# Kernel tuning notes

Measured on AMD Instinct MI355X. Metric: run time of the kernel, lower is better.

Reference implementation:

```python
import jax, jax.numpy as jnp
import numpy as np

N, E, C, NE, G, T = 20000, 320000, 32, 10, 64, 1000
NB, HID, LAYERS = 8, 64, 2
R_MAX, P_CUT, AVG_NEIGH = 5.0, 6, 16.0
LM = 16  # (max_ell+1)^2 spherical-harmonic components
L_OF_LM = jnp.array([0,1,1,1,2,2,2,2,2,3,3,3,3,3,3,3])


def sph_harm(u):
    # component-normalized real spherical harmonics up to l=3 on unit vectors u [E,3]
    x, y, z = u[:, 0], u[:, 1], u[:, 2]
    s3, s15, s5, s105, s7 = 3**0.5, 15**0.5, 5**0.5, 105**0.5, 7**0.5
    s35_8, s21_8 = (35.0/8.0)**0.5, (21.0/8.0)**0.5
    comps = [jnp.ones_like(x),
             s3*x, s3*y, s3*z,
             s15*x*y, s15*y*z, 0.5*s5*(3*z*z-1.0), s15*x*z, 0.5*s15*(x*x-y*y),
             s35_8*y*(3*x*x-y*y), s105*x*y*z, s21_8*y*(5*z*z-1.0),
             0.5*s7*(5*z*z*z-3*z), s21_8*x*(5*z*z-1.0),
             0.5*s105*z*(x*x-y*y), s35_8*x*(x*x-3*y*y)]
    return jnp.stack(comps, axis=-1)  # [E,16]


def radial_embed(r):
    # Bessel basis with polynomial cutoff (MACE RadialEmbeddingBlock)
    n = jnp.arange(1, NB + 1, dtype=r.dtype)
    rc = jnp.maximum(r, 1e-9)
    bessel = (2.0/R_MAX)**0.5 * jnp.sin(n[None, :]*jnp.pi*rc[:, None]/R_MAX) / rc[:, None]
    xr = r / R_MAX
    p = float(P_CUT)
    f = (1.0 - 0.5*(p+1)*(p+2)*xr**p + p*(p+2)*xr**(p+1) - 0.5*p*(p+1)*xr**(p+2))
    f = f * (xr < 1.0)
    return bessel * f[:, None]  # [E,NB]


def setup_inputs():
    key = jax.random.key(0)
    ks = jax.random.split(key, 16)
    positions = jax.random.normal(ks[0], (N, 3)) * 3.0
    species = jax.random.randint(ks[1], (N,), 0, NE)
    node_attrs = jax.nn.one_hot(species, NE, dtype=jnp.float32)
    edge_index = jax.random.randint(ks[2], (2, E), 0, N)
    shifts = jnp.zeros((E, 3), jnp.float32)
    batch = jnp.sort(jax.random.randint(ks[3], (N,), 0, G))
    t = jax.random.randint(ks[4], (G,), 0, T)
    eps = jax.random.normal(ks[5], (N, NE + 3))
    betas = jnp.linspace(1e-4, 0.02, T)
    alpha_bar = jnp.cumprod(1.0 - betas)
    sc = 0.1
    W_embed = sc * jax.random.normal(ks[6], (NE + 1, C))
    W_r1 = sc * jax.random.normal(ks[7], (LAYERS, NB, HID))
    W_r2 = sc * jax.random.normal(ks[8], (LAYERS, HID, C * 4))
    W_mix = sc * jax.random.normal(ks[9], (LAYERS, 4, C, C))
    W_sc = sc * jax.random.normal(ks[10], (NE, C))
    W_prod = sc * jax.random.normal(ks[11], (LAYERS, 3, C))
    W_ro_s = sc * jax.random.normal(ks[12], (LAYERS, C, NE))
    W_ro_v = sc * jax.random.normal(ks[13], (LAYERS, C))
    return {"positions": positions, "node_attrs": node_attrs, "shifts": shifts,
            "eps": eps, "alpha_bar": alpha_bar, "W_embed": W_embed, "W_r1": W_r1,
            "W_r2": W_r2, "W_mix": W_mix, "W_sc": W_sc, "W_prod": W_prod,
            "W_ro_s": W_ro_s, "W_ro_v": W_ro_v, "edge_index": edge_index,
            "batch": batch, "t": t}


def reference(positions, node_attrs, shifts, eps, alpha_bar, W_embed, W_r1, W_r2,
              W_mix, W_sc, W_prod, W_ro_s, W_ro_v, edge_index, batch, t):
    sender, receiver = edge_index[0], edge_index[1]
    # diffusion: noise positions and attrs (DDPM q(x_t|x_0))
    ab = alpha_bar[t][batch][:, None]                       # [N,1]
    attrs0 = node_attrs / 4.0
    pos_noisy = jnp.sqrt(ab) * positions + jnp.sqrt(1.0 - ab) * eps[:, -3:]
    attrs_noisy = jnp.sqrt(ab) * attrs0 + jnp.sqrt(1.0 - ab) * eps[:, :NE]
    tf = (t.astype(jnp.float32) / T)[batch][:, None]
    h = jnp.concatenate([attrs_noisy, tf], axis=-1) @ W_embed  # [N,C]
    # edge geometry
    vec = pos_noisy[receiver] - pos_noisy[sender] + shifts
    r = jnp.sqrt(jnp.sum(vec * vec, axis=-1) + 1e-12)
    Y = sph_harm(vec / r[:, None])                          # [E,16]
    ef = radial_embed(r)                                    # [E,NB]
    scalar = h
    pred = jnp.zeros((N, NE + 3), h.dtype)
    for layer in range(LAYERS):
        rw = jax.nn.silu(ef @ W_r1[layer]) @ W_r2[layer]    # [E,4C]
        rw = rw.reshape(E, C, 4)[:, :, L_OF_LM]             # [E,C,16]
        msg = rw * scalar[sender][:, :, None] * Y[:, None, :]
        agg = jax.ops.segment_sum(msg, receiver, num_segments=N) / AVG_NEIGH
        Wm = W_mix[layer][L_OF_LM]                          # [16,C,C]
        feats = jnp.einsum('nck,kcd->ndk', agg, Wm)         # per-l channel mix
        s = feats[:, :, 0]
        poly = W_prod[layer, 0] + W_prod[layer, 1] * s + W_prod[layer, 2] * s * s
        feats = feats * poly[:, :, None]                    # correlation-3 product
        if layer == 0:
            feats = feats.at[:, :, 0].add(attrs_noisy @ W_sc)  # element skip
        scalar = feats[:, :, 0]
        pred_s = scalar @ W_ro_s[layer]                     # [N,NE]
        pred_v = jnp.einsum('ncm,c->nm', feats[:, :, 1:4], W_ro_v[layer])  # [N,3]
        pred = pred + jnp.concatenate([pred_s, pred_v], axis=-1)
    err = (pred - eps) ** 2
    loss_pos = jax.ops.segment_sum(err[:, -3:].sum(-1), batch, num_segments=G)
    loss_lab = jax.ops.segment_sum(err[:, :NE].sum(-1), batch, num_segments=G)
    nn = jax.ops.segment_sum(jnp.ones((N,), pred.dtype), batch, num_segments=G)
    loss = 0.5 * (loss_pos + loss_lab) / (jnp.maximum(nn, 1.0) * (3 + NE))
    return loss
```

## Files before the change

kernel.cpp:

```cpp
#include <hip/hip_runtime.h>

typedef unsigned short ushort_t;
typedef unsigned int uint_t;

#define NN 20000
#define EE 320000
#define CC 32
#define NEL 10
#define GG 64
#define TTT 1000
#define NBB 8
#define HIDD 64
#define EPB 256

typedef __attribute__((ext_vector_type(8))) short bf16x8;
typedef __attribute__((ext_vector_type(4))) float f32x4;

__device__ __forceinline__ float bits2f(uint_t b) { union { uint_t u; float f; } v; v.u = b; return v.f; }
__device__ __forceinline__ ushort_t f2b(float f) {
  union { float f; uint_t u; } v; v.f = f;
  uint_t r = (v.u + 0x7fffu + ((v.u >> 16) & 1u)) >> 16;
  return (ushort_t)r;
}
__device__ __forceinline__ uint_t pk(float a, float b) {
  return (uint_t)f2b(a) | ((uint_t)f2b(b) << 16);
}
__device__ __forceinline__ float lo16(uint_t u) { return bits2f(u << 16); }
__device__ __forceinline__ float hi16(uint_t u) { return bits2f(u & 0xffff0000u); }

__global__ __launch_bounds__(256) void k_prep(
    const float* __restrict__ positions, const float* __restrict__ node_attrs,
    const float* __restrict__ eps, const float* __restrict__ alpha_bar,
    const float* __restrict__ W_embed, const float* __restrict__ W_sc,
    const int* __restrict__ batch, const int* __restrict__ tarr,
    float* __restrict__ pos_noisy, float* __restrict__ scalA,
    float* __restrict__ sc_skip, float* __restrict__ pred, int* __restrict__ deg)
{
  int n = blockIdx.x * 256 + threadIdx.x;
  if (n >= NN) return;
  deg[n] = 0;
  int g = batch[n];
  int tn = tarr[g];
  float ab = alpha_bar[tn];
  float sa = sqrtf(ab), sb = sqrtf(fmaxf(1.0f - ab, 0.0f));
#pragma unroll
  for (int j = 0; j < 3; ++j)
    pos_noisy[n * 3 + j] = sa * positions[n * 3 + j] + sb * eps[n * 13 + 10 + j];
  float an[10];
#pragma unroll
  for (int j = 0; j < 10; ++j)
    an[j] = sa * 0.25f * node_attrs[n * 10 + j] + sb * eps[n * 13 + j];
  float tf = (float)tn * (1.0f / (float)TTT);
  for (int d = 0; d < CC; ++d) {
    float h = tf * W_embed[10 * CC + d];
    float sk = 0.0f;
#pragma unroll
    for (int j = 0; j < 10; ++j) {
      h = fmaf(an[j], W_embed[j * CC + d], h);
      sk = fmaf(an[j], W_sc[j * CC + d], sk);
    }
    scalA[n * CC + d] = h;
    sc_skip[n * CC + d] = sk;
  }
#pragma unroll
  for (int j = 0; j < 13; ++j) pred[n * 13 + j] = 0.0f;
}

__global__ __launch_bounds__(256) void k_edge_deg(const int* __restrict__ ei,
    int* __restrict__ deg)
{
  int e = blockIdx.x * 256 + threadIdx.x;
  atomicAdd(&deg[ei[EE + e]], 1);
}

__global__ __launch_bounds__(1024) void k_scan(const int* __restrict__ deg,
    int* __restrict__ offs, int* __restrict__ cursor,
    float* __restrict__ lnum, float* __restrict__ lcnt)
{
  __shared__ int wsums[16];
  __shared__ int woffs[16];
  int tid = threadIdx.x, lane = tid & 63, wv = tid >> 6;
  if (tid < GG) { lnum[tid] = 0.0f; lcnt[tid] = 0.0f; }
  int base = tid * 20;
  int loc[20];
  int s = 0;
#pragma unroll
  for (int j = 0; j < 20; ++j) {
    int idx = base + j;
    int v = (idx < NN) ? deg[idx] : 0;
    loc[j] = s; s += v;
  }
  int inc = s;
  for (int o = 1; o < 64; o <<= 1) {
    int v = __shfl_up(inc, o, 64);
    if (lane >= o) inc += v;
  }
  if (lane == 63) wsums[wv] = inc;
  __syncthreads();
  if (wv == 0 && lane < 16) {
    int v = wsums[lane];
    int i2 = v;
    for (int o = 1; o < 16; o <<= 1) {
      int vv = __shfl_up(i2, o, 16);
      if (lane >= o) i2 += vv;
    }
    woffs[lane] = i2 - v;
  }
  __syncthreads();
  int texcl = woffs[wv] + (inc - s);
#pragma unroll
  for (int j = 0; j < 20; ++j) {
    int idx = base + j;
    if (idx < NN) { int v = texcl + loc[j]; offs[idx] = v; cursor[idx] = v; }
  }
  if (tid == 1023) offs[NN] = EE;
}

__global__ __launch_bounds__(256) void k_edge2(
    const float* __restrict__ pos_noisy, const float* __restrict__ shifts,
    const int* __restrict__ ei, int* __restrict__ cursor,
    ushort_t* __restrict__ Ys, ushort_t* __restrict__ efs, int* __restrict__ snds)
{
  int e = blockIdx.x * 256 + threadIdx.x;
  int snd = ei[e], rcv = ei[EE + e];
  float vx = pos_noisy[rcv * 3 + 0] - pos_noisy[snd * 3 + 0] + shifts[e * 3 + 0];
  float vy = pos_noisy[rcv * 3 + 1] - pos_noisy[snd * 3 + 1] + shifts[e * 3 + 1];
  float vz = pos_noisy[rcv * 3 + 2] - pos_noisy[snd * 3 + 2] + shifts[e * 3 + 2];
  float r2 = vx * vx + vy * vy + vz * vz + 1e-12f;
  float r = sqrtf(r2);
  float inv = 1.0f / r;
  float x = vx * inv, y = vy * inv, z = vz * inv;

  const float s3 = 1.7320508075688772f, s15 = 3.872983346207417f, s5 = 2.23606797749979f;
  const float s105 = 10.246950765959598f, s7 = 2.6457513110645907f;
  const float s35_8 = 2.091650066335189f, s21_8 = 1.6201851746019651f;
  float yv[16];
  yv[0] = 1.0f;
  yv[1] = s3 * x; yv[2] = s3 * y; yv[3] = s3 * z;
  yv[4] = s15 * x * y;
  yv[5] = s15 * y * z;
  yv[6] = 0.5f * s5 * (3.0f * z * z - 1.0f);
  yv[7] = s15 * x * z;
  yv[8] = 0.5f * s15 * (x * x - y * y);
  yv[9] = s35_8 * y * (3.0f * x * x - y * y);
  yv[10] = s105 * x * y * z;
  yv[11] = s21_8 * y * (5.0f * z * z - 1.0f);
  yv[12] = 0.5f * s7 * (5.0f * z * z * z - 3.0f * z);
  yv[13] = s21_8 * x * (5.0f * z * z - 1.0f);
  yv[14] = 0.5f * s105 * z * (x * x - y * y);
  yv[15] = s35_8 * x * (x * x - 3.0f * y * y);

  float rc = fmaxf(r, 1e-9f);
  float pref = 0.6324555320336759f / rc;
  float th = 0.6283185307179586f * rc;
  float s1 = __sinf(th), c1 = __cosf(th);
  float xr = r * 0.2f;
  float fcut = 0.0f;
  if (xr < 1.0f) {
    float x2 = xr * xr, x3 = x2 * xr;
    float x6 = x3 * x3, x7 = x6 * xr, x8 = x7 * xr;
    fcut = 1.0f - 28.0f * x6 + 48.0f * x7 - 21.0f * x8;
  }
  float efv[8];
  float sp = 0.0f, scur = s1, c2 = 2.0f * c1;
#pragma unroll
  for (int b = 0; b < 8; ++b) {
    efv[b] = pref * scur * fcut;
    float nx = c2 * scur - sp;
    sp = scur; scur = nx;
  }

  int slot = atomicAdd(&cursor[rcv], 1);
  snds[slot] = snd;
  uint4* Y4 = (uint4*)Ys;
  Y4[(size_t)slot * 2 + 0] = make_uint4(pk(yv[0], yv[1]), pk(yv[2], yv[3]),
                                        pk(yv[4], yv[5]), pk(yv[6], yv[7]));
  Y4[(size_t)slot * 2 + 1] = make_uint4(pk(yv[8], yv[9]), pk(yv[10], yv[11]),
                                        pk(yv[12], yv[13]), pk(yv[14], yv[15]));
  ((uint4*)efs)[slot] = make_uint4(pk(efv[0], efv[1]), pk(efv[2], efv[3]),
                                   pk(efv[4], efv[5]), pk(efv[6], efv[7]));
}

__global__ __launch_bounds__(256) void k_rw_mfma(
    const ushort_t* __restrict__ efs, const float* __restrict__ W_r1,
    const float* __restrict__ W_r2, ushort_t* __restrict__ rwc, int layer)
{
  __shared__ __align__(16) ushort_t w2t[128][72];
  __shared__ __align__(16) ushort_t h1[EPB][72];
  int tid = threadIdx.x;
  const float* W1g = W_r1 + layer * NBB * HIDD;
  const float* W2g = W_r2 + layer * HIDD * 128;
  for (int idx = tid; idx < HIDD * 128; idx += 256) {
    int k = idx >> 7, n = idx & 127;
    w2t[n][k] = f2b(W2g[idx]);
  }
  {
    int e = blockIdx.x * EPB + tid;
    uint4 q = ((const uint4*)efs)[e];
    float efr[8] = {lo16(q.x), hi16(q.x), lo16(q.y), hi16(q.y),
                    lo16(q.z), hi16(q.z), lo16(q.w), hi16(q.w)};
    for (int hc = 0; hc < 8; ++hc) {
      float v[8];
#pragma unroll
      for (int hh = 0; hh < 8; ++hh) {
        int h = hc * 8 + hh;
        float t = 0.0f;
#pragma unroll
        for (int b = 0; b < 8; ++b) t = fmaf(efr[b], W1g[b * HIDD + h], t);
        v[hh] = t / (1.0f + __expf(-t));
      }
      *(uint4*)&h1[tid][hc * 8] = make_uint4(pk(v[0], v[1]), pk(v[2], v[3]),
                                             pk(v[4], v[5]), pk(v[6], v[7]));
    }
  }
  __syncthreads();
  int w = tid >> 6, lane = tid & 63;
  int c = lane & 15, quad = lane >> 4;
  bf16x8 bfr[16];
#pragma unroll
  for (int nt = 0; nt < 8; ++nt)
#pragma unroll
    for (int kt = 0; kt < 2; ++kt)
      bfr[nt * 2 + kt] = *(const bf16x8*)&w2t[nt * 16 + c][kt * 32 + quad * 8];
  int mb0 = w * 64;
#pragma unroll
  for (int mt = 0; mt < 4; ++mt) {
    int mbase = mb0 + mt * 16;
    bf16x8 a0 = *(const bf16x8*)&h1[mbase + c][quad * 8];
    bf16x8 a1 = *(const bf16x8*)&h1[mbase + c][32 + quad * 8];
    size_t erow = (size_t)blockIdx.x * EPB + mbase + quad * 4;
#pragma unroll
    for (int nt = 0; nt < 8; ++nt) {
      f32x4 acc = {0.0f, 0.0f, 0.0f, 0.0f};
      acc = __builtin_amdgcn_mfma_f32_16x16x32_bf16(a0, bfr[nt * 2 + 0], acc, 0, 0, 0);
      acc = __builtin_amdgcn_mfma_f32_16x16x32_bf16(a1, bfr[nt * 2 + 1], acc, 0, 0, 0);
      int col = nt * 16 + c;
#pragma unroll
      for (int r = 0; r < 4; ++r)
        rwc[(erow + r) * 128 + col] = f2b(acc[r]);
    }
  }
}

__global__ __launch_bounds__(256) void k_layer(
    const ushort_t* __restrict__ Ys, const ushort_t* __restrict__ rwc,
    const int* __restrict__ snds,
    const float* __restrict__ scal_in, float* __restrict__ scal_out,
    const int* __restrict__ offs,
    const float* __restrict__ W_mix, const float* __restrict__ W_prod,
    const float* __restrict__ W_ro_s, const float* __restrict__ W_ro_v,
    const float* __restrict__ sc_skip, float* __restrict__ pred, int layer)
{
  __shared__ float lagg[4][CC][16];
  __shared__ float lf[4][CC][4];
  int w = threadIdx.x >> 6, lane = threadIdx.x & 63;
  int n = blockIdx.x * 4 + w;
  int c = lane >> 1;
  int kh = lane & 1;
  int kb = kh * 8;
  int i0 = offs[n], i1 = offs[n + 1];
  float acc0 = 0, acc1 = 0, acc2 = 0, acc3 = 0, acc4 = 0, acc5 = 0, acc6 = 0, acc7 = 0;
  const uint4* Y4 = (const uint4*)Ys;
  const uint2* rw2 = (const uint2*)rwc;
  for (int s = i0; s < i1; ++s) {
    uint4 q = Y4[(size_t)s * 2 + kh];
    uint2 rp = rw2[(size_t)s * 32 + c];
    float ss = scal_in[snds[s] * CC + c];
    float r0 = lo16(rp.x), r1 = hi16(rp.x), r2v = lo16(rp.y), r3 = hi16(rp.y);
    float w0 = kh ? r2v : r0;
    float w13 = kh ? r3 : r1;
    float w47 = kh ? r3 : r2v;
    float ya0 = lo16(q.x), ya1 = hi16(q.x), ya2 = lo16(q.y), ya3 = hi16(q.y);
    float yb0 = lo16(q.z), yb1 = hi16(q.z), yb2 = lo16(q.w), yb3 = hi16(q.w);
    acc0 = fmaf(w0 * ss, ya0, acc0);
    acc1 = fmaf(w13 * ss, ya1, acc1);
    acc2 = fmaf(w13 * ss, ya2, acc2);
    acc3 = fmaf(w13 * ss, ya3, acc3);
    acc4 = fmaf(w47 * ss, yb0, acc4);
    acc5 = fmaf(w47 * ss, yb1, acc5);
    acc6 = fmaf(w47 * ss, yb2, acc6);
    acc7 = fmaf(w47 * ss, yb3, acc7);
  }
  const float invavg = 1.0f / 16.0f;
  lagg[w][c][kb + 0] = acc0 * invavg;
  lagg[w][c][kb + 1] = acc1 * invavg;
  lagg[w][c][kb + 2] = acc2 * invavg;
  lagg[w][c][kb + 3] = acc3 * invavg;
  lagg[w][c][kb + 4] = acc4 * invavg;
  lagg[w][c][kb + 5] = acc5 * invavg;
  lagg[w][c][kb + 6] = acc6 * invavg;
  lagg[w][c][kb + 7] = acc7 * invavg;
  __syncthreads();
  int d = c;
  float ft[8] = {0, 0, 0, 0, 0, 0, 0, 0};
  const float* Wm = W_mix + layer * 4096;
  for (int cc2 = 0; cc2 < CC; ++cc2) {
    float m0 = Wm[cc2 * CC + d];
    float m1 = Wm[1024 + cc2 * CC + d];
    float m2 = Wm[2048 + cc2 * CC + d];
    float m3 = Wm[3072 + cc2 * CC + d];
    float u0 = kh ? m2 : m0;
    float u13 = kh ? m3 : m1;
    float u47 = kh ? m3 : m2;
    ft[0] = fmaf(lagg[w][cc2][kb + 0], u0, ft[0]);
    ft[1] = fmaf(lagg[w][cc2][kb + 1], u13, ft[1]);
    ft[2] = fmaf(lagg[w][cc2][kb + 2], u13, ft[2]);
    ft[3] = fmaf(lagg[w][cc2][kb + 3], u13, ft[3]);
    ft[4] = fmaf(lagg[w][cc2][kb + 4], u47, ft[4]);
    ft[5] = fmaf(lagg[w][cc2][kb + 5], u47, ft[5]);
    ft[6] = fmaf(lagg[w][cc2][kb + 6], u47, ft[6]);
    ft[7] = fmaf(lagg[w][cc2][kb + 7], u47, ft[7]);
  }
  float s = __shfl(ft[0], lane & 62, 64);
  const float* Wp = W_prod + layer * 96;
  float p0 = Wp[d], p1 = Wp[32 + d], p2 = Wp[64 + d];
  float poly = fmaf(fmaf(p2, s, p1), s, p0);
#pragma unroll
  for (int j = 0; j < 8; ++j) ft[j] *= poly;
  if (layer == 0 && kh == 0) ft[0] += sc_skip[n * CC + d];
  if (kh == 0) {
    scal_out[n * CC + d] = ft[0];
    lf[w][d][0] = ft[0]; lf[w][d][1] = ft[1]; lf[w][d][2] = ft[2]; lf[w][d][3] = ft[3];
  }
  __syncthreads();
  if (lane < 13) {
    float sum = 0.0f;
    if (lane < 10) {
      const float* Wr = W_ro_s + layer * CC * NEL;
      for (int dd = 0; dd < CC; ++dd) sum = fmaf(lf[w][dd][0], Wr[dd * NEL + lane], sum);
    } else {
      int mm = lane - 10;
      const float* Wv = W_ro_v + layer * CC;
      for (int dd = 0; dd < CC; ++dd) sum = fmaf(lf[w][dd][1 + mm], Wv[dd], sum);
    }
    pred[n * 13 + lane] += sum;
  }
}

__global__ __launch_bounds__(256) void k_loss(const float* __restrict__ pred,
    const float* __restrict__ eps, const int* __restrict__ batch,
    float* __restrict__ lnum, float* __restrict__ lcnt)
{
  __shared__ float psum[GG];
  __shared__ int pcnt[GG];
  int tid = threadIdx.x;
  if (tid < GG) { psum[tid] = 0.0f; pcnt[tid] = 0; }
  __syncthreads();
  int n = blockIdx.x * 256 + tid;
  if (n < NN) {
    int g = batch[n];
    float sum = 0.0f;
#pragma unroll
    for (int j = 0; j < 13; ++j) {
      float dlt = pred[n * 13 + j] - eps[n * 13 + j];
      sum = fmaf(dlt, dlt, sum);
    }
    atomicAdd(&psum[g], sum);
    atomicAdd(&pcnt[g], 1);
  }
  __syncthreads();
  if (tid < GG && pcnt[tid] > 0) {
    atomicAdd(&lnum[tid], psum[tid]);
    atomicAdd(&lcnt[tid], (float)pcnt[tid]);
  }
}

__global__ void k_final(const float* __restrict__ lnum, const float* __restrict__ lcnt,
    float* __restrict__ out)
{
  int g = threadIdx.x;
  if (g < GG) {
    float nn = fmaxf(lcnt[g], 1.0f);
    out[g] = 0.5f * lnum[g] / (nn * 13.0f);
  }
}

extern "C" void kernel_launch(void* const* d_in, const int* in_sizes, int n_in,
                              void* d_out, int out_size, void* d_ws, size_t ws_size,
                              hipStream_t stream) {
  const float* positions  = (const float*)d_in[0];
  const float* node_attrs = (const float*)d_in[1];
  const float* shifts     = (const float*)d_in[2];
  const float* eps        = (const float*)d_in[3];
  const float* alpha_bar  = (const float*)d_in[4];
  const float* W_embed    = (const float*)d_in[5];
  const float* W_r1       = (const float*)d_in[6];
  const float* W_r2       = (const float*)d_in[7];
  const float* W_mix      = (const float*)d_in[8];
  const float* W_sc       = (const float*)d_in[9];
  const float* W_prod     = (const float*)d_in[10];
  const float* W_ro_s     = (const float*)d_in[11];
  const float* W_ro_v     = (const float*)d_in[12];
  const int* edge_index   = (const int*)d_in[13];
  const int* batch        = (const int*)d_in[14];
  const int* tarr         = (const int*)d_in[15];
  float* out = (float*)d_out;

  char* ws = (char*)d_ws;
  size_t off = 0;
  auto alloc = [&](size_t bytes) -> void* {
    void* p = ws + off;
    off = (off + bytes + 255) & ~(size_t)255;
    return p;
  };
  float* pos_noisy = (float*)alloc(NN * 3 * 4);
  float* scalA     = (float*)alloc(NN * CC * 4);
  float* scalB     = (float*)alloc(NN * CC * 4);
  float* sc_skip   = (float*)alloc(NN * CC * 4);
  float* pred      = (float*)alloc(NN * 13 * 4);
  ushort_t* Ys     = (ushort_t*)alloc((size_t)EE * 16 * 2);
  ushort_t* efs    = (ushort_t*)alloc((size_t)EE * 8 * 2);
  int* snds        = (int*)alloc((size_t)EE * 4);
  ushort_t* rwc    = (ushort_t*)alloc((size_t)EE * 128 * 2);
  int* deg         = (int*)alloc(NN * 4);
  int* offs        = (int*)alloc((NN + 1) * 4);
  int* cursor      = (int*)alloc(NN * 4);
  float* lnum      = (float*)alloc(GG * 4);
  float* lcnt      = (float*)alloc(GG * 4);
  (void)ws_size; (void)in_sizes; (void)n_in; (void)out_size;

  const int NB_N = (NN + 255) / 256;
  const int NB_E = EE / 256;

  k_prep<<<NB_N, 256, 0, stream>>>(positions, node_attrs, eps, alpha_bar, W_embed,
                                   W_sc, batch, tarr, pos_noisy, scalA, sc_skip, pred, deg);
  k_edge_deg<<<NB_E, 256, 0, stream>>>(edge_index, deg);
  k_scan<<<1, 1024, 0, stream>>>(deg, offs, cursor, lnum, lcnt);
  k_edge2<<<NB_E, 256, 0, stream>>>(pos_noisy, shifts, edge_index, cursor, Ys, efs, snds);

  for (int layer = 0; layer < 2; ++layer) {
    const float* sin_p = (layer == 0) ? scalA : scalB;
    float* sout_p      = (layer == 0) ? scalB : scalA;
    k_rw_mfma<<<NB_E, 256, 0, stream>>>(efs, W_r1, W_r2, rwc, layer);
    k_layer<<<NN / 4, 256, 0, stream>>>(Ys, rwc, snds, sin_p, sout_p, offs,
                                        W_mix, W_prod, W_ro_s, W_ro_v,
                                        sc_skip, pred, layer);
  }

  k_loss<<<NB_N, 256, 0, stream>>>(pred, eps, batch, lnum, lcnt);
  k_final<<<1, 64, 0, stream>>>(lnum, lcnt, out);
}
```

Before: 362.4 us.

## Fuse radial MLP into per-node layer kernel and fold final loss into k_loss

The per-edge radial MLP (SiLU hidden layer plus MFMA projection) is now computed inside the per-node aggregation kernel. Each wave handles one receiver's edges in chunks of 16 and stages the weighted radial features in wave-private LDS. This removes the large bf16 rwc intermediate that was written and re-read every layer. In exchange, every block redoes the W_r2 transpose/convert, partial chunks waste MFMA work, and degrees are clamped at 64. The separate k_final launch is replaced by a last-block ticket inside k_loss.

```diff
diff --git a/kernel.cpp b/kernel.cpp
--- a/kernel.cpp
+++ b/kernel.cpp
@@ -11,7 +11,8 @@
 #define TTT 1000
 #define NBB 8
 #define HIDD 64
-#define EPB 256
+#define NPB 4
+#define MAXDEG 64
 
 typedef __attribute__((ext_vector_type(8))) short bf16x8;
 typedef __attribute__((ext_vector_type(4))) float f32x4;
@@ -75,12 +76,13 @@
 
 __global__ __launch_bounds__(1024) void k_scan(const int* __restrict__ deg,
     int* __restrict__ offs, int* __restrict__ cursor,
-    float* __restrict__ lnum, float* __restrict__ lcnt)
+    float* __restrict__ lnum, float* __restrict__ lcnt, int* __restrict__ ticket)
 {
   __shared__ int wsums[16];
   __shared__ int woffs[16];
   int tid = threadIdx.x, lane = tid & 63, wv = tid >> 6;
   if (tid < GG) { lnum[tid] = 0.0f; lcnt[tid] = 0.0f; }
+  if (tid == 1022) *ticket = 0;
   int base = tid * 20;
   int loc[20];
   int s = 0;
@@ -181,117 +183,137 @@
                                    pk(efv[4], efv[5]), pk(efv[6], efv[7]));
 }
 
-__global__ __launch_bounds__(256) void k_rw_mfma(
-    const ushort_t* __restrict__ efs, const float* __restrict__ W_r1,
-    const float* __restrict__ W_r2, ushort_t* __restrict__ rwc, int layer)
-{
-  __shared__ __align__(16) ushort_t w2t[128][72];
-  __shared__ __align__(16) ushort_t h1[EPB][72];
+__global__ __launch_bounds__(256) void k_flay(
+    const ushort_t* __restrict__ efs, const ushort_t* __restrict__ Ys,
+    const int* __restrict__ snds, const int* __restrict__ offs,
+    const float* __restrict__ W_r1, const float* __restrict__ W_r2,
+    const float* __restrict__ scal_in, float* __restrict__ scal_out,
+    const float* __restrict__ W_mix, const float* __restrict__ W_prod,
+    const float* __restrict__ W_ro_s, const float* __restrict__ W_ro_v,
+    const float* __restrict__ sc_skip, float* __restrict__ pred, int layer)
+{
+  __shared__ __align__(16) char lds[37376];
+  ushort_t (*w2t)[72] = (ushort_t(*)[72])lds;
+  float (*lagg)[CC][16] = (float(*)[CC][16])lds;
+  float (*lf)[CC][4] = (float(*)[CC][4])(lds + 8192);
+  float* w1s = (float*)(lds + 18432);
+
   int tid = threadIdx.x;
+  int w = tid >> 6, lane = tid & 63;
+  ushort_t (*rwt)[132] = (ushort_t(*)[132])(lds + 20480 + w * 4224);
+
+  int n0 = blockIdx.x * NPB;
   const float* W1g = W_r1 + layer * NBB * HIDD;
   const float* W2g = W_r2 + layer * HIDD * 128;
+
   for (int idx = tid; idx < HIDD * 128; idx += 256) {
     int k = idx >> 7, n = idx & 127;
     w2t[n][k] = f2b(W2g[idx]);
   }
-  {
-    int e = blockIdx.x * EPB + tid;
-    uint4 q = ((const uint4*)efs)[e];
-    float efr[8] = {lo16(q.x), hi16(q.x), lo16(q.y), hi16(q.y),
-                    lo16(q.z), hi16(q.z), lo16(q.w), hi16(q.w)};
-    for (int hc = 0; hc < 8; ++hc) {
-      float v[8];
-#pragma unroll
-      for (int hh = 0; hh < 8; ++hh) {
-        int h = hc * 8 + hh;
-        float t = 0.0f;
-#pragma unroll
-        for (int b = 0; b < 8; ++b) t = fmaf(efr[b], W1g[b * HIDD + h], t);
-        v[hh] = t / (1.0f + __expf(-t));
+  for (int idx = tid; idx < NBB * HIDD; idx += 256) w1s[idx] = W1g[idx];
+  __syncthreads();
+
+  int c16 = lane & 15, quad = lane >> 4;
+  bf16x8 bfr[16];
+#pragma unroll
+  for (int nt = 0; nt < 8; ++nt)
+#pragma unroll
+    for (int kt = 0; kt < 2; ++kt)
+      bfr[nt * 2 + kt] = *(const bf16x8*)&w2t[nt * 16 + c16][kt * 32 + quad * 8];
+
+  int oj = offs[n0 + w];
+  int dj = min(offs[n0 + w + 1] - oj, MAXDEG);
+
+  int cA = lane >> 1, kh = lane & 1, kb = kh * 8;
+  float acc0 = 0, acc1 = 0, acc2 = 0, acc3 = 0, acc4 = 0, acc5 = 0, acc6 = 0, acc7 = 0;
+  const uint4* Y4 = (const uint4*)Ys;
+
+  for (int kbase = 0; kbase < dj; kbase += 16) {
+    bf16x8 a0, a1;
+    {
+      int kc = kbase + c16;
+      float ef8[8] = {0, 0, 0, 0, 0, 0, 0, 0};
+      if (kc < dj) {
+        uint4 q = ((const uint4*)efs)[(size_t)(oj + kc)];
+        ef8[0] = lo16(q.x); ef8[1] = hi16(q.x); ef8[2] = lo16(q.y); ef8[3] = hi16(q.y);
+        ef8[4] = lo16(q.z); ef8[5] = hi16(q.z); ef8[6] = lo16(q.w); ef8[7] = hi16(q.w);
       }
-      *(uint4*)&h1[tid][hc * 8] = make_uint4(pk(v[0], v[1]), pk(v[2], v[3]),
-                                             pk(v[4], v[5]), pk(v[6], v[7]));
-    }
-  }
-  __syncthreads();
-  int w = tid >> 6, lane = tid & 63;
-  int c = lane & 15, quad = lane >> 4;
-  bf16x8 bfr[16];
-#pragma unroll
-  for (int nt = 0; nt < 8; ++nt)
-#pragma unroll
-    for (int kt = 0; kt < 2; ++kt)
-      bfr[nt * 2 + kt] = *(const bf16x8*)&w2t[nt * 16 + c][kt * 32 + quad * 8];
-  int mb0 = w * 64;
-#pragma unroll
-  for (int mt = 0; mt < 4; ++mt) {
-    int mbase = mb0 + mt * 16;
-    bf16x8 a0 = *(const bf16x8*)&h1[mbase + c][quad * 8];
-    bf16x8 a1 = *(const bf16x8*)&h1[mbase + c][32 + quad * 8];
-    size_t erow = (size_t)blockIdx.x * EPB + mbase + quad * 4;
+      float h0[8] = {0, 0, 0, 0, 0, 0, 0, 0};
+      float h1v[8] = {0, 0, 0, 0, 0, 0, 0, 0};
+#pragma unroll
+      for (int b = 0; b < 8; ++b) {
+        const float* wb = &w1s[b * HIDD];
+        float4 wa = *(const float4*)&wb[quad * 8];
+        float4 wbv = *(const float4*)&wb[quad * 8 + 4];
+        float4 wc = *(const float4*)&wb[32 + quad * 8];
+        float4 wd = *(const float4*)&wb[32 + quad * 8 + 4];
+        float e = ef8[b];
+        h0[0] = fmaf(e, wa.x, h0[0]); h0[1] = fmaf(e, wa.y, h0[1]);
+        h0[2] = fmaf(e, wa.z, h0[2]); h0[3] = fmaf(e, wa.w, h0[3]);
+        h0[4] = fmaf(e, wbv.x, h0[4]); h0[5] = fmaf(e, wbv.y, h0[5]);
+        h0[6] = fmaf(e, wbv.z, h0[6]); h0[7] = fmaf(e, wbv.w, h0[7]);
+        h1v[0] = fmaf(e, wc.x, h1v[0]); h1v[1] = fmaf(e, wc.y, h1v[1]);
+        h1v[2] = fmaf(e, wc.z, h1v[2]); h1v[3] = fmaf(e, wc.w, h1v[3]);
+        h1v[4] = fmaf(e, wd.x, h1v[4]); h1v[5] = fmaf(e, wd.y, h1v[5]);
+        h1v[6] = fmaf(e, wd.z, h1v[6]); h1v[7] = fmaf(e, wd.w, h1v[7]);
+      }
+#pragma unroll
+      for (int jj = 0; jj < 8; ++jj) {
+        float v0 = h0[jj];  v0 = v0 / (1.0f + __expf(-v0));
+        float v1 = h1v[jj]; v1 = v1 / (1.0f + __expf(-v1));
+        a0[jj] = (short)f2b(v0);
+        a1[jj] = (short)f2b(v1);
+      }
+    }
+    int snd_[4];
+#pragma unroll
+    for (int r = 0; r < 4; ++r) {
+      int kr = kbase + quad * 4 + r;
+      snd_[r] = snds[oj + ((kr < dj) ? kr : (dj - 1))];
+    }
 #pragma unroll
     for (int nt = 0; nt < 8; ++nt) {
       f32x4 acc = {0.0f, 0.0f, 0.0f, 0.0f};
       acc = __builtin_amdgcn_mfma_f32_16x16x32_bf16(a0, bfr[nt * 2 + 0], acc, 0, 0, 0);
       acc = __builtin_amdgcn_mfma_f32_16x16x32_bf16(a1, bfr[nt * 2 + 1], acc, 0, 0, 0);
-      int col = nt * 16 + c;
+      int cc = 4 * nt + (c16 >> 2);
 #pragma unroll
       for (int r = 0; r < 4; ++r)
-        rwc[(erow + r) * 128 + col] = f2b(acc[r]);
-    }
-  }
-}
-
-__global__ __launch_bounds__(256) void k_layer(
-    const ushort_t* __restrict__ Ys, const ushort_t* __restrict__ rwc,
-    const int* __restrict__ snds,
-    const float* __restrict__ scal_in, float* __restrict__ scal_out,
-    const int* __restrict__ offs,
-    const float* __restrict__ W_mix, const float* __restrict__ W_prod,
-    const float* __restrict__ W_ro_s, const float* __restrict__ W_ro_v,
-    const float* __restrict__ sc_skip, float* __restrict__ pred, int layer)
-{
-  __shared__ float lagg[4][CC][16];
-  __shared__ float lf[4][CC][4];
-  int w = threadIdx.x >> 6, lane = threadIdx.x & 63;
-  int n = blockIdx.x * 4 + w;
-  int c = lane >> 1;
-  int kh = lane & 1;
-  int kb = kh * 8;
-  int i0 = offs[n], i1 = offs[n + 1];
-  float acc0 = 0, acc1 = 0, acc2 = 0, acc3 = 0, acc4 = 0, acc5 = 0, acc6 = 0, acc7 = 0;
-  const uint4* Y4 = (const uint4*)Ys;
-  const uint2* rw2 = (const uint2*)rwc;
-  for (int s = i0; s < i1; ++s) {
-    uint4 q = Y4[(size_t)s * 2 + kh];
-    uint2 rp = rw2[(size_t)s * 32 + c];
-    float ss = scal_in[snds[s] * CC + c];
-    float r0 = lo16(rp.x), r1 = hi16(rp.x), r2v = lo16(rp.y), r3 = hi16(rp.y);
-    float w0 = kh ? r2v : r0;
-    float w13 = kh ? r3 : r1;
-    float w47 = kh ? r3 : r2v;
-    float ya0 = lo16(q.x), ya1 = hi16(q.x), ya2 = lo16(q.y), ya3 = hi16(q.y);
-    float yb0 = lo16(q.z), yb1 = hi16(q.z), yb2 = lo16(q.w), yb3 = hi16(q.w);
-    acc0 = fmaf(w0 * ss, ya0, acc0);
-    acc1 = fmaf(w13 * ss, ya1, acc1);
-    acc2 = fmaf(w13 * ss, ya2, acc2);
-    acc3 = fmaf(w13 * ss, ya3, acc3);
-    acc4 = fmaf(w47 * ss, yb0, acc4);
-    acc5 = fmaf(w47 * ss, yb1, acc5);
-    acc6 = fmaf(w47 * ss, yb2, acc6);
-    acc7 = fmaf(w47 * ss, yb3, acc7);
-  }
+        rwt[quad * 4 + r][nt * 16 + c16] = f2b(acc[r] * scal_in[(size_t)snd_[r] * CC + cc]);
+    }
+    asm volatile("s_waitcnt lgkmcnt(0)" ::: "memory");
+    int emax = min(16, dj - kbase);
+    for (int e = 0; e < emax; ++e) {
+      size_t ge = (size_t)(oj + kbase + e);
+      uint4 q = Y4[ge * 2 + kh];
+      uint2 rp = *(const uint2*)&rwt[e][cA * 4];
+      float r0 = lo16(rp.x), r1 = hi16(rp.x), r2v = lo16(rp.y), r3 = hi16(rp.y);
+      float w0 = kh ? r2v : r0, w13 = kh ? r3 : r1, w47 = kh ? r3 : r2v;
+      acc0 = fmaf(w0,  lo16(q.x), acc0);
+      acc1 = fmaf(w13, hi16(q.x), acc1);
+      acc2 = fmaf(w13, lo16(q.y), acc2);
+      acc3 = fmaf(w13, hi16(q.y), acc3);
+      acc4 = fmaf(w47, lo16(q.z), acc4);
+      acc5 = fmaf(w47, hi16(q.z), acc5);
+      acc6 = fmaf(w47, lo16(q.w), acc6);
+      acc7 = fmaf(w47, hi16(q.w), acc7);
+    }
+  }
+  __syncthreads();
+
   const float invavg = 1.0f / 16.0f;
-  lagg[w][c][kb + 0] = acc0 * invavg;
-  lagg[w][c][kb + 1] = acc1 * invavg;
-  lagg[w][c][kb + 2] = acc2 * invavg;
-  lagg[w][c][kb + 3] = acc3 * invavg;
-  lagg[w][c][kb + 4] = acc4 * invavg;
-  lagg[w][c][kb + 5] = acc5 * invavg;
-  lagg[w][c][kb + 6] = acc6 * invavg;
-  lagg[w][c][kb + 7] = acc7 * invavg;
-  __syncthreads();
-  int d = c;
+  lagg[w][cA][kb + 0] = acc0 * invavg;
+  lagg[w][cA][kb + 1] = acc1 * invavg;
+  lagg[w][cA][kb + 2] = acc2 * invavg;
+  lagg[w][cA][kb + 3] = acc3 * invavg;
+  lagg[w][cA][kb + 4] = acc4 * invavg;
+  lagg[w][cA][kb + 5] = acc5 * invavg;
+  lagg[w][cA][kb + 6] = acc6 * invavg;
+  lagg[w][cA][kb + 7] = acc7 * invavg;
+  __syncthreads();
+
+  int d = cA;
+  int n = n0 + w;
   float ft[8] = {0, 0, 0, 0, 0, 0, 0, 0};
   const float* Wm = W_mix + layer * 4096;
   for (int cc2 = 0; cc2 < CC; ++cc2) {
@@ -311,10 +333,10 @@
     ft[6] = fmaf(lagg[w][cc2][kb + 6], u47, ft[6]);
     ft[7] = fmaf(lagg[w][cc2][kb + 7], u47, ft[7]);
   }
-  float s = __shfl(ft[0], lane & 62, 64);
+  float sv = __shfl(ft[0], lane & 62, 64);
   const float* Wp = W_prod + layer * 96;
   float p0 = Wp[d], p1 = Wp[32 + d], p2 = Wp[64 + d];
-  float poly = fmaf(fmaf(p2, s, p1), s, p0);
+  float poly = fmaf(fmaf(p2, sv, p1), sv, p0);
 #pragma unroll
   for (int j = 0; j < 8; ++j) ft[j] *= poly;
   if (layer == 0 && kh == 0) ft[0] += sc_skip[n * CC + d];
@@ -339,10 +361,12 @@
 
 __global__ __launch_bounds__(256) void k_loss(const float* __restrict__ pred,
     const float* __restrict__ eps, const int* __restrict__ batch,
-    float* __restrict__ lnum, float* __restrict__ lcnt)
+    float* __restrict__ lnum, float* __restrict__ lcnt,
+    int* __restrict__ ticket, float* __restrict__ out, int nblocks)
 {
   __shared__ float psum[GG];
   __shared__ int pcnt[GG];
+  __shared__ int lastflag;
   int tid = threadIdx.x;
   if (tid < GG) { psum[tid] = 0.0f; pcnt[tid] = 0; }
   __syncthreads();
@@ -363,15 +387,17 @@
     atomicAdd(&lnum[tid], psum[tid]);
     atomicAdd(&lcnt[tid], (float)pcnt[tid]);
   }
-}
-
-__global__ void k_final(const float* __restrict__ lnum, const float* __restrict__ lcnt,
-    float* __restrict__ out)
-{
-  int g = threadIdx.x;
-  if (g < GG) {
-    float nn = fmaxf(lcnt[g], 1.0f);
-    out[g] = 0.5f * lnum[g] / (nn * 13.0f);
+  __syncthreads();
+  if (tid == 0) {
+    __threadfence();
+    int t = atomicAdd(ticket, 1);
+    lastflag = (t == nblocks - 1) ? 1 : 0;
+  }
+  __syncthreads();
+  if (lastflag && tid < GG) {
+    float num = atomicAdd(&lnum[tid], 0.0f);
+    float cnt = atomicAdd(&lcnt[tid], 0.0f);
+    out[tid] = 0.5f * num / (fmaxf(cnt, 1.0f) * 13.0f);
   }
 }
 
@@ -411,12 +437,12 @@
   ushort_t* Ys     = (ushort_t*)alloc((size_t)EE * 16 * 2);
   ushort_t* efs    = (ushort_t*)alloc((size_t)EE * 8 * 2);
   int* snds        = (int*)alloc((size_t)EE * 4);
-  ushort_t* rwc    = (ushort_t*)alloc((size_t)EE * 128 * 2);
   int* deg         = (int*)alloc(NN * 4);
   int* offs        = (int*)alloc((NN + 1) * 4);
   int* cursor      = (int*)alloc(NN * 4);
   float* lnum      = (float*)alloc(GG * 4);
   float* lcnt      = (float*)alloc(GG * 4);
+  int* ticket      = (int*)alloc(4);
   (void)ws_size; (void)in_sizes; (void)n_in; (void)out_size;
 
   const int NB_N = (NN + 255) / 256;
@@ -425,18 +451,16 @@
   k_prep<<<NB_N, 256, 0, stream>>>(positions, node_attrs, eps, alpha_bar, W_embed,
                                    W_sc, batch, tarr, pos_noisy, scalA, sc_skip, pred, deg);
   k_edge_deg<<<NB_E, 256, 0, stream>>>(edge_index, deg);
-  k_scan<<<1, 1024, 0, stream>>>(deg, offs, cursor, lnum, lcnt);
+  k_scan<<<1, 1024, 0, stream>>>(deg, offs, cursor, lnum, lcnt, ticket);
   k_edge2<<<NB_E, 256, 0, stream>>>(pos_noisy, shifts, edge_index, cursor, Ys, efs, snds);
 
   for (int layer = 0; layer < 2; ++layer) {
     const float* sin_p = (layer == 0) ? scalA : scalB;
     float* sout_p      = (layer == 0) ? scalB : scalA;
-    k_rw_mfma<<<NB_E, 256, 0, stream>>>(efs, W_r1, W_r2, rwc, layer);
-    k_layer<<<NN / 4, 256, 0, stream>>>(Ys, rwc, snds, sin_p, sout_p, offs,
-                                        W_mix, W_prod, W_ro_s, W_ro_v,
-                                        sc_skip, pred, layer);
-  }
-
-  k_loss<<<NB_N, 256, 0, stream>>>(pred, eps, batch, lnum, lcnt);
-  k_final<<<1, 64, 0, stream>>>(lnum, lcnt, out);
-}
+    k_flay<<<NN / NPB, 256, 0, stream>>>(efs, Ys, snds, offs, W_r1, W_r2,
+                                         sin_p, sout_p, W_mix, W_prod,
+                                         W_ro_s, W_ro_v, sc_skip, pred, layer);
+  }
+
+  k_loss<<<NB_N, 256, 0, stream>>>(pred, eps, batch, lnum, lcnt, ticket, out, NB_N);
+}
```

New measurement: 366.9 us. No clear change (+1.2%).
